# Optimization experiments

Measured on AMD Instinct MI355X. Metric: run time of the kernel, lower is better.

Reference implementation:

```python
import jax, jax.numpy as jnp
import numpy as np

B, N_CLS, M_TIME, U_LAB = 1024, 96, 256, 40


def setup_inputs() -> dict:
    key = jax.random.key(0)
    k1, k2, k3 = jax.random.split(key, 3)
    logits = jax.random.normal(k1, (B, N_CLS, M_TIME), dtype=jnp.float32)
    # module treats inputs as per-timestep class probabilities (softmax output of CRNN)
    out_padded = jax.nn.softmax(logits, axis=1)
    label = jax.random.randint(k2, (B, U_LAB), 1, N_CLS, dtype=jnp.int32)  # 0 is blank
    unpadded_w = jax.random.randint(k3, (B,), 512, 4 * M_TIME + 1, dtype=jnp.int32)
    return {"out_padded": out_padded, "label": label, "unpadded_w": unpadded_w}


def _alpha(probs, lab, T, L):
    # probs: (M, N) time-major class probabilities; lab: (U,) label indices; T traced int.
    # Faithful to compute_alpha: per-timestep renormalization over [start, end),
    # recurrence computed for s in [start, L).
    M = probs.shape[0]
    s_idx = jnp.arange(L)
    i_idx = jnp.maximum((s_idx - 1) // 2, 0)
    is_odd = (s_idx % 2) == 1
    cls = jnp.where(is_odd, lab[i_idx], 0)  # blank = class 0 for even s
    # skip (a[t-1][s-2]) allowed only for odd s != 1 with non-repeated label
    skip = is_odd & (s_idx != 1) & (lab[i_idx] != lab[jnp.maximum(i_idx - 1, 0)])

    p0 = probs[0]
    row0 = jnp.zeros((L,), probs.dtype).at[0].set(p0[0]).at[1].set(p0[lab[0]])
    c0 = row0[0] + row0[1]
    row0 = jnp.where((s_idx < 2) & (c0 > 0), row0 / jnp.where(c0 > 0, c0, 1.0), row0)

    def step(prev, t):
        start = jnp.maximum(0, L - 2 * (T - t))
        end = jnp.minimum(2 * t + 2, L)
        pm1 = jnp.concatenate([jnp.zeros((1,), prev.dtype), prev[:-1]])
        pm2 = jnp.concatenate([jnp.zeros((2,), prev.dtype), prev[:-2]])
        val = (prev
               + jnp.where(s_idx > 0, pm1, 0.0)
               + jnp.where(skip, pm2, 0.0)) * probs[t, cls]
        val = jnp.where(s_idx >= start, val, 0.0)  # s < start stays zero
        nmask = (s_idx >= start) & (s_idx < end)
        c = jnp.sum(jnp.where(nmask, val, 0.0))
        val = jnp.where(nmask & (c > 0), val / jnp.where(c > 0, c, 1.0), val)
        return val, val

    _, rows = jax.lax.scan(step, row0, jnp.arange(1, M))
    a = jnp.concatenate([row0[None, :], rows], axis=0)  # (M, L)
    return jnp.where((jnp.arange(M) < T)[:, None], a, 0.0)  # rows >= T are zero


def _ctc_single(out_cw, lab, w):
    probs = out_cw.T  # (M, N): time x classes, as in torch.transpose(out, 1, 0)
    M = probs.shape[0]
    U = lab.shape[0]
    L = 2 * U + 1
    T = w // 4
    a = _alpha(probs, lab, T, L)
    # 'beta' faithful to source: alpha on CLASS-flipped probs (torch.fliplr on (T,N))
    # with reversed labels, then flipud+fliplr of the (T,L) result.
    b_raw = _alpha(probs[:, ::-1], lab[::-1], T, L)
    src = T - 1 - jnp.arange(M)
    valid = (src >= 0) & (src < M)
    b = jnp.where(valid[:, None], b_raw[jnp.clip(src, 0, M - 1)], 0.0)[:, ::-1]
    ab = a * b  # (M, L)
    s_idx = jnp.arange(L)
    cls = jnp.where((s_idx % 2) == 1, lab[jnp.maximum((s_idx - 1) // 2, 0)], 0)
    lh = jnp.sum(ab / probs[:, cls], axis=1)  # (M,)
    tmask = jnp.arange(M) < T
    return -jnp.sum(jnp.where(tmask, jnp.log(jnp.where(tmask, lh, 1.0)), 0.0))


def reference(out_padded, label, unpadded_w):
    losses = jax.vmap(_ctc_single)(out_padded, label, unpadded_w)  # (B,)
    return jnp.sum(losses)
```

## Files before the change

### kernel.cpp

```cpp
#include <hip/hip_runtime.h>
#include <cmath>

namespace {
constexpr int BN = 1024;
constexpr int NC = 96;
constexpr int MT = 256;
constexpr int UL = 40;
constexpr int LS = 81;
constexpr int PAIRS = 41;

template <int CTRL>
__device__ __forceinline__ float dppf(float v) {
  return __builtin_bit_cast(
      float, __builtin_amdgcn_update_dpp(0, __builtin_bit_cast(int, v), CTRL,
                                         0xf, 0xf, true));
}
__device__ __forceinline__ float rl63(float x) {
  return __builtin_bit_cast(
      float, __builtin_amdgcn_readlane(__builtin_bit_cast(int, x), 63));
}
__device__ __forceinline__ float wave_sum(float x) {
  x += dppf<0x111>(x);
  x += dppf<0x112>(x);
  x += dppf<0x114>(x);
  x += dppf<0x118>(x);
  x += dppf<0x142>(x);
  x += dppf<0x143>(x);
  return rl63(x);
}
__device__ __forceinline__ float wave_shr1(float v) { return dppf<0x138>(v); }
__device__ __forceinline__ float fast_rcp(float x) {
  return __builtin_amdgcn_rcpf(x);
}
__device__ __forceinline__ unsigned packu(float a, float b) {
  unsigned ua = __builtin_bit_cast(unsigned, a) >> 16;
  unsigned ub = __builtin_bit_cast(unsigned, b) & 0xffff0000u;
  return ua | ub;
}
__device__ __forceinline__ float bf_lo(unsigned u) {
  return __builtin_bit_cast(float, u << 16);
}
__device__ __forceinline__ float bf_hi(unsigned u) {
  return __builtin_bit_cast(float, u & 0xffff0000u);
}

constexpr float FQ = 1e8f;
constexpr float SEPS = 1e-30f;

__global__ __launch_bounds__(64) void chain_kernel(
    const float* __restrict__ gout, const int* __restrict__ glabel,
    const int* __restrict__ gw, unsigned* __restrict__ xa,
    unsigned* __restrict__ xb) {
  const int bx = blockIdx.x;
  const int b = bx >> 1, ph = bx & 1;
  const int i = threadIdx.x;
  const float* P = gout + (size_t)b * (NC * MT);
  const int* lab = glabel + b * UL;
  const int T = gw[b] >> 2;

  const int s0 = 2 * i, s1 = s0 + 1;
  const float h0f = (i <= 40) ? 1.f : 0.f;
  const float h1f = (i <= 39) ? 1.f : 0.f;
  const int iw = (i <= 40) ? i : 40;
  const bool act = (i <= 40);

  const float* pB;
  const float* pL;
  float mskf;
  unsigned* outp;
  if (ph == 0) {
    const int li = (i < UL) ? lab[i] : 0;
    const int lm = (i >= 1 && i < UL) ? lab[i - 1] : 0;
    pB = P;
    pL = P + (size_t)li * MT;
    mskf = (i >= 1 && i <= 39 && li != lm) ? 1.f : 0.f;
    outp = xa + (size_t)b * MT * PAIRS + iw;
  } else {
    const int rli = (i < UL) ? lab[UL - 1 - i] : 0;
    const int rlm = (i >= 1 && i < UL) ? lab[UL - i] : 0;
    pB = P + (size_t)(NC - 1) * MT;
    pL = P + (size_t)(NC - 1 - rli) * MT;
    mskf = (i >= 1 && i <= 39 && rli != rlm) ? 1.f : 0.f;
    outp = xb + (size_t)b * MT * PAIRS + (40 - iw);
  }

  float pbv[8], plv[8];
  float4 LA = *(const float4*)(pB + 0), LB = *(const float4*)(pB + 4);
  float4 MA = *(const float4*)(pL + 0), MB = *(const float4*)(pL + 4);
  pbv[0] = LA.x; pbv[1] = LA.y; pbv[2] = LA.z; pbv[3] = LA.w;
  pbv[4] = LB.x; pbv[5] = LB.y; pbv[6] = LB.z; pbv[7] = LB.w;
  plv[0] = MA.x; plv[1] = MA.y; plv[2] = MA.z; plv[3] = MA.w;
  plv[4] = MB.x; plv[5] = MB.y; plv[6] = MB.z; plv[7] = MB.w;
  LA = *(const float4*)(pB + 8); LB = *(const float4*)(pB + 12);
  MA = *(const float4*)(pL + 8); MB = *(const float4*)(pL + 12);

  float v0 = (i == 0) ? pbv[0] : 0.f;
  float v1 = (i == 0) ? plv[0] : 0.f;

  float f0[8], f1[8], sv[8];
  if (ph == 0) {
    sv[0] = v0 + v1;
    f0[0] = (i == 0) ? 1.f : 0.f;
    f1[0] = f0[0];
    v0 *= FQ;
    v1 *= FQ;
  } else {
    v0 *= FQ;
    v1 *= FQ;
    sv[0] = v0 + v1;
    f0[0] = v0;
    f1[0] = 0.f;
  }

#define CTC_STEP(T_, K_, DOMASK)                                      \
  {                                                                   \
    float pm1 = wave_shr1(v1);                                        \
    if (ph == 1 && (K_) >= 1) f1[(K_)-1] = pm1;                       \
    float u0 = v0 + pm1;                                              \
    float u1 = (v0 + v1) + pm1 * mskf;                                \
    if (DOMASK) {                                                     \
      const int start_ = LS - 2 * (T - (T_));                         \
      if (s0 < start_) u0 = 0.f;                                      \
      if (s1 < start_) u1 = 0.f;                                      \
    }                                                                 \
    const float x0 = u0 * h0f, x1 = u1 * h1f;                         \
    float n0 = x0 * pbv[(K_)];                                        \
    float n1 = x1 * plv[(K_)];                                        \
    sv[(K_)] = n0 + n1;                                               \
    v0 = n0; v1 = n1;                                                 \
    if (ph == 0) { f0[(K_)] = x0; f1[(K_)] = x1; }                    \
    else { f0[(K_)] = n0; }                                           \
  }

#define WS_LEVEL(CTRL)                                                \
  {                                                                   \
    _Pragma("unroll")                                                 \
    for (int k = 0; k < 8; ++k) sv[k] += dppf<CTRL>(sv[k]);           \
  }

#define CTC_BURST(T0_)                                                \
  {                                                                   \
    if (ph == 1) f1[7] = wave_shr1(v1);          \
    WS_LEVEL(0x111) WS_LEVEL(0x112) WS_LEVEL(0x114)                   \
    WS_LEVEL(0x118) WS_LEVEL(0x142) WS_LEVEL(0x143)                   \
    _Pragma("unroll")                                                 \
    for (int k = 0; k < 8; ++k) sv[k] = rl63(sv[k]);                  \
    if (act) {                                                        \
      unsigned ob[8];                                                 \
      _Pragma("unroll")                                               \
      for (int k = 0; k < 8; ++k) {                                   \
        float inv = fast_rcp(fmaxf(sv[k], SEPS));                     \
        ob[k] = packu(f0[k] * inv, f1[k] * inv);                      \
      }                                                               \
      if ((T0_) + 7 < T) {                                            \
        _Pragma("unroll")                                             \
        for (int k = 0; k < 8; ++k)                                   \
          outp[((T0_) + k) * PAIRS] = ob[k];      \
      } else {                                                        \
        _Pragma("unroll")                                             \
        for (int k = 0; k < 8; ++k)                                   \
          if ((T0_) + k < T) outp[((T0_) + k) * PAIRS] = ob[k];       \
      }                                                               \
    }                                                                 \
    float rb = FQ * fast_rcp(fmaxf(sv[7], SEPS));                     \
    rb = fminf(fmaxf(rb, 1e-20f), 1e20f);                             \
    v0 *= rb; v1 *= rb;                                               \
  }

#define CTC_UNPACK()                                                  \
  {                                                                   \
    pbv[0] = LA.x; pbv[1] = LA.y; pbv[2] = LA.z; pbv[3] = LA.w;       \
    pbv[4] = LB.x; pbv[5] = LB.y; pbv[6] = LB.z; pbv[7] = LB.w;       \
    plv[0] = MA.x; plv[1] = MA.y; plv[2] = MA.z; plv[3] = MA.w;       \
    plv[4] = MB.x; plv[5] = MB.y; plv[6] = MB.z; plv[7] = MB.w;       \
    int np = t0 + 8;                                                  \
    if (np > 248) np = 248;                                           \
    LA = *(const float4*)(pB + np); LB = *(const float4*)(pB + np + 4); \
    MA = *(const float4*)(pL + np); MB = *(const float4*)(pL + np + 4); \
  }

#pragma unroll
  for (int k = 1; k < 8; ++k) CTC_STEP(k, k, false);
  CTC_BURST(0);

  int t0 = 8;
  for (; t0 + 47 < T; t0 += 8) {
    CTC_UNPACK();
#pragma unroll
    for (int k = 0; k < 8; ++k) CTC_STEP(t0 + k, k, false);
    CTC_BURST(t0);
  }
  for (; t0 < T; t0 += 8) {
    CTC_UNPACK();
#pragma unroll
    for (int k = 0; k < 8; ++k) CTC_STEP(t0 + k, k, true);
    CTC_BURST(t0);
  }
#undef CTC_STEP
#undef CTC_BURST
#undef CTC_UNPACK
#undef WS_LEVEL
}

__global__ __launch_bounds__(256) void combine_kernel(
    const int* __restrict__ gw, const unsigned* __restrict__ xa,
    const unsigned* __restrict__ xb, float* __restrict__ loss_out) {
  const int b = blockIdx.x;
  const int tid = threadIdx.x;
  const int T = gw[b] >> 2;
  float lsum = 0.f;
  if (tid < T) {
    const unsigned* A = xa + ((size_t)b * MT + tid) * PAIRS;
    const unsigned* Bb = xb + ((size_t)b * MT + (T - 1 - tid)) * PAIRS;
    float d = 0.f;
#pragma unroll
    for (int p = 0; p < PAIRS; ++p) {
      const unsigned av = A[p];
      const unsigned bv = Bb[p];
      d = fmaf(bf_lo(av), bf_lo(bv), d);
      d = fmaf(bf_hi(av), bf_hi(bv), d);
    }
    lsum = -__logf(fmaxf(d, 1e-37f));
  }
  lsum = wave_sum(lsum);
  __shared__ float part[4];
  if ((tid & 63) == 0) part[tid >> 6] = lsum;
  __syncthreads();
  if (tid == 0) {
    float L = part[0] + part[1] + part[2] + part[3];
    loss_out[b] = fminf(fmaxf(L, -1e30f), 1e30f);
  }
}

__global__ void reduce_kernel(const float* __restrict__ loss_in,
                              float* __restrict__ out) {
  __shared__ double sm[256];
  const int tid = threadIdx.x;
  double s = 0.0;
  for (int k = tid; k < BN; k += 256) s += (double)loss_in[k];
  sm[tid] = s;
  __syncthreads();
  for (int w = 128; w >= 1; w >>= 1) {
    if (tid < w) sm[tid] += sm[tid + w];
    __syncthreads();
  }
  if (tid == 0) out[0] = (float)sm[0];
}
}

extern "C" void kernel_launch(void* const* d_in, const int* in_sizes, int n_in,
                              void* d_out, int out_size, void* d_ws, size_t ws_size,
                              hipStream_t stream) {
  const float* gout = (const float*)d_in[0];
  const int* glabel = (const int*)d_in[1];
  const int* gw = (const int*)d_in[2];
  unsigned* xa = (unsigned*)d_ws;
  unsigned* xb = xa + (size_t)BN * MT * PAIRS;
  float* loss = (float*)(xb + (size_t)BN * MT * PAIRS);
  chain_kernel<<<2 * BN, 64, 0, stream>>>(gout, glabel, gw, xa, xb);
  combine_kernel<<<BN, 256, 0, stream>>>(gw, xa, xb, loss);
  reduce_kernel<<<1, 256, 0, stream>>>(loss, (float*)d_out);
}
```

Baseline: 190.6 us.

## Widen CTC renormalization burst to 16 timesteps with a mid-burst scale boost

```diff
diff --git a/kernel.cpp b/kernel.cpp
--- a/kernel.cpp
+++ b/kernel.cpp
@@ -46,6 +46,7 @@
 
 constexpr float FQ = 1e8f;
 constexpr float SEPS = 1e-30f;
+constexpr float GB = 1099511627776.0f;
 
 __global__ __launch_bounds__(64) void chain_kernel(
     const float* __restrict__ gout, const int* __restrict__ glabel,
@@ -84,20 +85,28 @@
     outp = xb + (size_t)b * MT * PAIRS + (40 - iw);
   }
 
-  float pbv[8], plv[8];
-  float4 LA = *(const float4*)(pB + 0), LB = *(const float4*)(pB + 4);
-  float4 MA = *(const float4*)(pL + 0), MB = *(const float4*)(pL + 4);
-  pbv[0] = LA.x; pbv[1] = LA.y; pbv[2] = LA.z; pbv[3] = LA.w;
-  pbv[4] = LB.x; pbv[5] = LB.y; pbv[6] = LB.z; pbv[7] = LB.w;
-  plv[0] = MA.x; plv[1] = MA.y; plv[2] = MA.z; plv[3] = MA.w;
-  plv[4] = MB.x; plv[5] = MB.y; plv[6] = MB.z; plv[7] = MB.w;
-  LA = *(const float4*)(pB + 8); LB = *(const float4*)(pB + 12);
-  MA = *(const float4*)(pL + 8); MB = *(const float4*)(pL + 12);
+  float pbv[16], plv[16];
+  float4 LA = *(const float4*)(pB + 0),  LB = *(const float4*)(pB + 4);
+  float4 LC = *(const float4*)(pB + 8),  LD = *(const float4*)(pB + 12);
+  float4 MA = *(const float4*)(pL + 0),  MB = *(const float4*)(pL + 4);
+  float4 MC = *(const float4*)(pL + 8),  MD = *(const float4*)(pL + 12);
+  pbv[0] = LA.x;  pbv[1] = LA.y;  pbv[2] = LA.z;  pbv[3] = LA.w;
+  pbv[4] = LB.x;  pbv[5] = LB.y;  pbv[6] = LB.z;  pbv[7] = LB.w;
+  pbv[8] = LC.x;  pbv[9] = LC.y;  pbv[10] = LC.z; pbv[11] = LC.w;
+  pbv[12] = LD.x; pbv[13] = LD.y; pbv[14] = LD.z; pbv[15] = LD.w;
+  plv[0] = MA.x;  plv[1] = MA.y;  plv[2] = MA.z;  plv[3] = MA.w;
+  plv[4] = MB.x;  plv[5] = MB.y;  plv[6] = MB.z;  plv[7] = MB.w;
+  plv[8] = MC.x;  plv[9] = MC.y;  plv[10] = MC.z; plv[11] = MC.w;
+  plv[12] = MD.x; plv[13] = MD.y; plv[14] = MD.z; plv[15] = MD.w;
+  LA = *(const float4*)(pB + 16); LB = *(const float4*)(pB + 20);
+  LC = *(const float4*)(pB + 24); LD = *(const float4*)(pB + 28);
+  MA = *(const float4*)(pL + 16); MB = *(const float4*)(pL + 20);
+  MC = *(const float4*)(pL + 24); MD = *(const float4*)(pL + 28);
 
   float v0 = (i == 0) ? pbv[0] : 0.f;
   float v1 = (i == 0) ? plv[0] : 0.f;
 
-  float f0[8], f1[8], sv[8];
+  float f0[16], f1[16], sv[16];
   if (ph == 0) {
     sv[0] = v0 + v1;
     f0[0] = (i == 0) ? 1.f : 0.f;
@@ -112,10 +121,11 @@
     f1[0] = 0.f;
   }
 
-#define CTC_STEP(T_, K_, DOMASK)                                      \
+#define CTC_STEP(T_, K_, DOMASK, BOOST)                               \
   {                                                                   \
     float pm1 = wave_shr1(v1);                                        \
     if (ph == 1 && (K_) >= 1) f1[(K_)-1] = pm1;                       \
+    if (BOOST) { v0 *= GB; v1 *= GB; pm1 *= GB; }                     \
     float u0 = v0 + pm1;                                              \
     float u1 = (v0 + v1) + pm1 * mskf;                                \
     if (DOMASK) {                                                     \
@@ -135,65 +145,80 @@
 #define WS_LEVEL(CTRL)                                                \
   {                                                                   \
     _Pragma("unroll")                                                 \
-    for (int k = 0; k < 8; ++k) sv[k] += dppf<CTRL>(sv[k]);           \
+    for (int k = 0; k < 16; ++k) sv[k] += dppf<CTRL>(sv[k]);          \
   }
 
 #define CTC_BURST(T0_)                                                \
   {                                                                   \
-    if (ph == 1) f1[7] = wave_shr1(v1);          \
+    if (ph == 1) f1[15] = wave_shr1(v1);         \
     WS_LEVEL(0x111) WS_LEVEL(0x112) WS_LEVEL(0x114)                   \
     WS_LEVEL(0x118) WS_LEVEL(0x142) WS_LEVEL(0x143)                   \
     _Pragma("unroll")                                                 \
-    for (int k = 0; k < 8; ++k) sv[k] = rl63(sv[k]);                  \
+    for (int k = 0; k < 16; ++k) sv[k] = rl63(sv[k]);                 \
     if (act) {                                                        \
-      unsigned ob[8];                                                 \
+      unsigned ob[16];                                                \
       _Pragma("unroll")                                               \
-      for (int k = 0; k < 8; ++k) {                                   \
+      for (int k = 0; k < 16; ++k) {                                  \
         float inv = fast_rcp(fmaxf(sv[k], SEPS));                     \
         ob[k] = packu(f0[k] * inv, f1[k] * inv);                      \
       }                                                               \
-      if ((T0_) + 7 < T) {                                            \
+      if ((T0_) + 15 < T) {                                           \
         _Pragma("unroll")                                             \
-        for (int k = 0; k < 8; ++k)                                   \
+        for (int k = 0; k < 16; ++k)                                  \
           outp[((T0_) + k) * PAIRS] = ob[k];      \
       } else {                                                        \
         _Pragma("unroll")                                             \
-        for (int k = 0; k < 8; ++k)                                   \
+        for (int k = 0; k < 16; ++k)                                  \
           if ((T0_) + k < T) outp[((T0_) + k) * PAIRS] = ob[k];       \
       }                                                               \
     }                                                                 \
-    float rb = FQ * fast_rcp(fmaxf(sv[7], SEPS));                     \
+    float rb = FQ * fast_rcp(fmaxf(sv[15], SEPS));                    \
     rb = fminf(fmaxf(rb, 1e-20f), 1e20f);                             \
     v0 *= rb; v1 *= rb;                                               \
   }
 
-#define CTC_UNPACK()                                                  \
-  {                                                                   \
-    pbv[0] = LA.x; pbv[1] = LA.y; pbv[2] = LA.z; pbv[3] = LA.w;       \
-    pbv[4] = LB.x; pbv[5] = LB.y; pbv[6] = LB.z; pbv[7] = LB.w;       \
-    plv[0] = MA.x; plv[1] = MA.y; plv[2] = MA.z; plv[3] = MA.w;       \
-    plv[4] = MB.x; plv[5] = MB.y; plv[6] = MB.z; plv[7] = MB.w;       \
-    int np = t0 + 8;                                                  \
-    if (np > 248) np = 248;                                           \
-    LA = *(const float4*)(pB + np); LB = *(const float4*)(pB + np + 4); \
-    MA = *(const float4*)(pL + np); MB = *(const float4*)(pL + np + 4); \
-  }
-
-#pragma unroll
-  for (int k = 1; k < 8; ++k) CTC_STEP(k, k, false);
+#define CTC_UNPACK(T0_)                                               \
+  {                                                                   \
+    pbv[0] = LA.x;  pbv[1] = LA.y;  pbv[2] = LA.z;  pbv[3] = LA.w;    \
+    pbv[4] = LB.x;  pbv[5] = LB.y;  pbv[6] = LB.z;  pbv[7] = LB.w;    \
+    pbv[8] = LC.x;  pbv[9] = LC.y;  pbv[10] = LC.z; pbv[11] = LC.w;   \
+    pbv[12] = LD.x; pbv[13] = LD.y; pbv[14] = LD.z; pbv[15] = LD.w;   \
+    plv[0] = MA.x;  plv[1] = MA.y;  plv[2] = MA.z;  plv[3] = MA.w;    \
+    plv[4] = MB.x;  plv[5] = MB.y;  plv[6] = MB.z;  plv[7] = MB.w;    \
+    plv[8] = MC.x;  plv[9] = MC.y;  plv[10] = MC.z; plv[11] = MC.w;   \
+    plv[12] = MD.x; plv[13] = MD.y; plv[14] = MD.z; plv[15] = MD.w;   \
+    int np = (T0_) + 16;                                              \
+    if (np > 240) np = 240;                                           \
+    LA = *(const float4*)(pB + np);      LB = *(const float4*)(pB + np + 4);  \
+    LC = *(const float4*)(pB + np + 8);  LD = *(const float4*)(pB + np + 12); \
+    MA = *(const float4*)(pL + np);      MB = *(const float4*)(pL + np + 4);  \
+    MC = *(const float4*)(pL + np + 8);  MD = *(const float4*)(pL + np + 12); \
+  }
+
+#pragma unroll
+  for (int k = 1; k < 8; ++k) CTC_STEP(k, k, false, 0);
+  CTC_STEP(8, 8, false, 1);
+#pragma unroll
+  for (int k = 9; k < 16; ++k) CTC_STEP(k, k, false, 0);
   CTC_BURST(0);
 
-  int t0 = 8;
-  for (; t0 + 47 < T; t0 += 8) {
-    CTC_UNPACK();
-#pragma unroll
-    for (int k = 0; k < 8; ++k) CTC_STEP(t0 + k, k, false);
+  int t0 = 16;
+  for (; t0 + 56 <= T; t0 += 16) {
+    CTC_UNPACK(t0);
+#pragma unroll
+    for (int k = 0; k < 8; ++k) CTC_STEP(t0 + k, k, false, 0);
+    CTC_STEP(t0 + 8, 8, false, 1);
+#pragma unroll
+    for (int k = 9; k < 16; ++k) CTC_STEP(t0 + k, k, false, 0);
     CTC_BURST(t0);
   }
-  for (; t0 < T; t0 += 8) {
-    CTC_UNPACK();
-#pragma unroll
-    for (int k = 0; k < 8; ++k) CTC_STEP(t0 + k, k, true);
+  for (; t0 < T; t0 += 16) {
+    CTC_UNPACK(t0);
+#pragma unroll
+    for (int k = 0; k < 8; ++k) CTC_STEP(t0 + k, k, true, 0);
+    CTC_STEP(t0 + 8, 8, true, 1);
+#pragma unroll
+    for (int k = 9; k < 16; ++k) CTC_STEP(t0 + k, k, true, 0);
     CTC_BURST(t0);
   }
 #undef CTC_STEP
```

Measured after the change: 183.9 us (median of 2 runs). 1.04x faster.
